# Kernel optimization log

Hardware: AMD Instinct MI355X
Metric: run time of the kernel (lower is better)

## Reference

```python
import jax, jax.numpy as jnp
import numpy as np
from jax import lax

GAMMA = 1.0
INF = 1000000.0  # matches the TF code's pseudo-infinity


def _pairwise_sq_dists(a, b):
    # ||a_i - b_j||^2 = ||a||^2 + ||b||^2 - 2 a.b ; avoids the [B,N,M,d] diff tensor
    a2 = jnp.sum(a * a, axis=-1)                      # (B, N)
    b2 = jnp.sum(b * b, axis=-1)                      # (B, M)
    ab = jnp.einsum('bnd,bmd->bnm', a, b)             # (B, N, M)
    return a2[:, :, None] + b2[:, None, :] - 2.0 * ab


def _soft_dtw(seq_a, seq_b, gamma):
    D = _pairwise_sq_dists(seq_a, seq_b)              # (B, N, M)
    B, N, M = D.shape
    dtype = D.dtype
    # row 0 of the DP table: R[0,0]=0, R[0,j>0]=INF
    row0 = jnp.full((B, M + 1), INF, dtype=dtype).at[:, 0].set(0.0)

    def row_step(prev_row, d_i):
        # prev_row: (B, M+1) = R[i-1, :]; d_i: (B, M) = D[:, i-1, :]
        def col_step(left, inputs):
            diag, up, d = inputs                      # each (B,)
            r = jnp.stack([diag, up, left], axis=-1)  # (B, 3)
            softmin = -gamma * jax.nn.logsumexp(-r / gamma, axis=-1)
            val = d + softmin
            return val, val
        left0 = jnp.full((B,), INF, dtype=dtype)      # R[i, 0] = INF
        xs = (prev_row[:, :-1].T, prev_row[:, 1:].T, d_i.T)  # scan over M
        _, vals = lax.scan(col_step, left0, xs)       # (M, B)
        new_row = jnp.concatenate([jnp.full((B, 1), INF, dtype=dtype), vals.T], axis=1)
        return new_row, None

    final_row, _ = lax.scan(row_step, row0, jnp.moveaxis(D, 1, 0))
    return final_row[:, -1]                           # R[N, M]


def setup_inputs() -> dict:
    key = jax.random.key(0)
    k1, k2 = jax.random.split(key)
    B, N, M, d = 128, 384, 384, 128
    seq_a = jax.random.normal(k1, (B, N, d), dtype=jnp.float32)
    seq_b = jax.random.normal(k2, (B, M, d), dtype=jnp.float32)
    return {"seq_a": seq_a, "seq_b": seq_b}


def reference(seq_a, seq_b):
    dist = _soft_dtw(seq_a, seq_b, GAMMA)
    return dist[:, None]                              # (B, 1)
```

## Files before the change

### kernel.cpp

```cpp
#include <hip/hip_runtime.h>
#include <stdint.h>

#define BATCH 128
#define SEQN  384
#define SEQM  384
#define DIM   128
#define KINF   1000000.0f
#define LOG2E  1.4426950408889634f
#define LN2    0.6931471805599453f
#define KINF2  (KINF * LOG2E)

#define RING    204
#define RSTRIDE 392

#define EXP2F(x) __builtin_amdgcn_exp2f(x)
#define LOG2F(x) __builtin_amdgcn_logf(x)

#define WG __HIP_MEMORY_SCOPE_WORKGROUP

typedef __attribute__((ext_vector_type(8))) short bf16x8;
typedef __attribute__((ext_vector_type(4))) float f32x4;

__device__ __forceinline__ unsigned short bf16_rne(float x) {
    uint32_t u = __float_as_uint(x);
    u += 0x7FFFu + ((u >> 16) & 1u);
    return (unsigned short)(u >> 16);
}
__device__ __forceinline__ uint32_t bf16_pair(float x, float y) {
    uint32_t ux = __float_as_uint(x); ux += 0x7FFFu + ((ux >> 16) & 1u);
    uint32_t uy = __float_as_uint(y); uy += 0x7FFFu + ((uy >> 16) & 1u);
    return (ux >> 16) | (uy & 0xFFFF0000u);
}

union frag_u { bf16x8 v; uint32_t u[4]; };

__global__ __launch_bounds__(512) void fused_dtw(
        const float* __restrict__ A, const float* __restrict__ B,
        float* __restrict__ out) {
    __shared__ __align__(16) unsigned short ring[RING * RSTRIDE];
    __shared__ __align__(16) float normA[SEQN];
    __shared__ int prod_done[16];
    __shared__ int cons_pp;

    const int bat  = blockIdx.x;
    const int tid  = threadIdx.x;
    const int wv   = tid >> 6;
    const int lane = tid & 63;

    if (tid < 16) prod_done[tid] = 0;
    if (tid == 16) cons_pp = -1;
    __syncthreads();

    if (wv == 4) {
        int g = 0;
        while (__hip_atomic_load(&cons_pp, __ATOMIC_ACQUIRE, WG) < 84) {
            __builtin_amdgcn_s_sleep(8);
            if (++g > (1 << 20)) break;
        }
        uint32_t pv = bf16_pair(KINF2, KINF2);
        #pragma unroll
        for (int c = 0; c < 4; c++) {
            uint32_t* p = (uint32_t*)&ring[(384 - RING + c) * RSTRIDE + 6 * lane];
            p[0] = pv; p[1] = pv; p[2] = pv;
        }
        if (lane == 0)
            __hip_atomic_fetch_add(&prod_done[12], 6, __ATOMIC_RELEASE, WG);
        return;
    }

    if (wv != 0) {
        const int pidx  = (wv < 4) ? (wv - 1) : (wv - 2);
        const int sbase = pidx * 4;
        const int l16 = lane & 15, q = lane >> 4;
        const float* __restrict__ Ab = A + (long)bat * SEQN * DIM;
        const float* __restrict__ Bb = B + (long)bat * SEQM * DIM;
        bool first = true;
        for (int k = 0; k < 12; k++) {
            if (k >= 6) {
                int thr = 8 * k - 12, g = 0;
                while (__hip_atomic_load(&cons_pp, __ATOMIC_ACQUIRE, WG) < thr) {
                    __builtin_amdgcn_s_sleep(2);
                    if (++g > (1 << 21)) break;
                }
            }
            frag_u bfrag[2][4];
            float bn[2];
            #pragma unroll
            for (int jg = 0; jg < 2; jg++) {
                const float* bp = Bb + (long)(32 * k + jg * 16 + l16) * DIM + q * 8;
                float s = 0.0f;
                #pragma unroll
                for (int kk = 0; kk < 4; kk++) {
                    float4 v0 = *(const float4*)(bp + kk * 32);
                    float4 v1 = *(const float4*)(bp + kk * 32 + 4);
                    bfrag[jg][kk].u[0] = bf16_pair(v0.x, v0.y);
                    bfrag[jg][kk].u[1] = bf16_pair(v0.z, v0.w);
                    bfrag[jg][kk].u[2] = bf16_pair(v1.x, v1.y);
                    bfrag[jg][kk].u[3] = bf16_pair(v1.z, v1.w);
                    s += v0.x*v0.x + v0.y*v0.y + v0.z*v0.z + v0.w*v0.w
                       + v1.x*v1.x + v1.y*v1.y + v1.z*v1.z + v1.w*v1.w;
                }
                s += __shfl_xor(s, 16, 64);
                s += __shfl_xor(s, 32, 64);
                bn[jg] = s;
            }
            float4 c0v[4], c1v[4];
            {
                const float* ap = Ab + (long)(sbase * 16 + l16) * DIM + q * 8;
                #pragma unroll
                for (int kk = 0; kk < 4; kk++) {
                    c0v[kk] = *(const float4*)(ap + kk * 32);
                    c1v[kk] = *(const float4*)(ap + kk * 32 + 4);
                }
            }
            #pragma unroll
            for (int s4 = 0; s4 < 4; s4++) {
                const int si = sbase + s4;
                float4 n0[4], n1[4];
                if (s4 < 3) {
                    const float* ap = Ab + (long)((si + 1) * 16 + l16) * DIM + q * 8;
                    #pragma unroll
                    for (int kk = 0; kk < 4; kk++) {
                        n0[kk] = *(const float4*)(ap + kk * 32);
                        n1[kk] = *(const float4*)(ap + kk * 32 + 4);
                    }
                }
                frag_u afr[4];
                #pragma unroll
                for (int kk = 0; kk < 4; kk++) {
                    afr[kk].u[0] = bf16_pair(c0v[kk].x, c0v[kk].y);
                    afr[kk].u[1] = bf16_pair(c0v[kk].z, c0v[kk].w);
                    afr[kk].u[2] = bf16_pair(c1v[kk].x, c1v[kk].y);
                    afr[kk].u[3] = bf16_pair(c1v[kk].z, c1v[kk].w);
                }
                if (first) {
                    float sa = 0.0f;
                    #pragma unroll
                    for (int kk = 0; kk < 4; kk++)
                        sa += c0v[kk].x*c0v[kk].x + c0v[kk].y*c0v[kk].y
                            + c0v[kk].z*c0v[kk].z + c0v[kk].w*c0v[kk].w
                            + c1v[kk].x*c1v[kk].x + c1v[kk].y*c1v[kk].y
                            + c1v[kk].z*c1v[kk].z + c1v[kk].w*c1v[kk].w;
                    sa += __shfl_xor(sa, 16, 64);
                    sa += __shfl_xor(sa, 32, 64);
                    if (q == 0) normA[si * 16 + l16] = sa;
                }
                f32x4 acc0 = {0.0f, 0.0f, 0.0f, 0.0f};
                f32x4 acc1 = {0.0f, 0.0f, 0.0f, 0.0f};
                #pragma unroll
                for (int kk = 0; kk < 4; kk++) {
                    acc0 = __builtin_amdgcn_mfma_f32_16x16x32_bf16(
                               afr[kk].v, bfrag[0][kk].v, acc0, 0, 0, 0);
                    acc1 = __builtin_amdgcn_mfma_f32_16x16x32_bf16(
                               afr[kk].v, bfrag[1][kk].v, acc1, 0, 0, 0);
                }
                if (first) asm volatile("s_waitcnt lgkmcnt(0)" ::: "memory");
                float4 an = *(const float4*)&normA[si * 16 + q * 4];
                #pragma unroll
                for (int jg = 0; jg < 2; jg++) {
                    int col  = 32 * k + jg * 16 + l16;
                    int slot = col >= RING ? col - RING : col;
                    f32x4 ac = jg ? acc1 : acc0;
                    ushort4 pk;
                    pk.x = bf16_rne((an.x + bn[jg] - 2.0f * ac[0]) * LOG2E);
                    pk.y = bf16_rne((an.y + bn[jg] - 2.0f * ac[1]) * LOG2E);
                    pk.z = bf16_rne((an.z + bn[jg] - 2.0f * ac[2]) * LOG2E);
                    pk.w = bf16_rne((an.w + bn[jg] - 2.0f * ac[3]) * LOG2E);
                    *(ushort4*)&ring[slot * RSTRIDE + si * 16 + q * 4] = pk;
                }
                if (s4 < 3) {
                    #pragma unroll
                    for (int kk = 0; kk < 4; kk++) { c0v[kk] = n0[kk]; c1v[kk] = n1[kk]; }
                }
            }
            first = false;
            if (lane == 0)
                __hip_atomic_fetch_add(&prod_done[k], 1, __ATOMIC_RELEASE, WG);
        }
        return;
    }

    const int t = lane;
    {
        int g = 0;
        while (__hip_atomic_load(&prod_done[0], __ATOMIC_ACQUIRE, WG) < 6)
            if (++g > (1 << 22)) break;
    }
    __builtin_amdgcn_s_setprio(1);
    const unsigned short* __restrict__ ringT = ring + 6 * t;

    float prev[6];
    #pragma unroll
    for (int r = 0; r < 6; r++) prev[r] = KINF2;

    uint3 dslot[4];
    #pragma unroll
    for (int qq = 0; qq < 4; qq++) {
        int c = qq - 2 * t;
        int cc = c < 0 ? 0 : c;
        dslot[qq] = *(const uint3*)(ringT + (long)cc * RSTRIDE);
    }

    float rcv0 = KINF2, rcv1 = KINF2, old_diag = KINF2;
    float lane0_diag = 0.0f;
    const bool isl0 = (t == 0);
    int c0 = -2 * t;

#define UNPACK(d, w)                                                        \
    d[0] = __uint_as_float(w.x << 16);                                      \
    d[1] = __uint_as_float(w.x & 0xFFFF0000u);                              \
    d[2] = __uint_as_float(w.y << 16);                                      \
    d[3] = __uint_as_float(w.y & 0xFFFF0000u);                              \
    d[4] = __uint_as_float(w.z << 16);                                      \
    d[5] = __uint_as_float(w.z & 0xFFFF0000u);

#define COLPASS(dX, diag0, upseed, LEFTV, NEWV)                             \
    {                                                                       \
        float Bp = (upseed), Fp = 1.0f;                                     \
        float Bv[6], Fv[6];                                                 \
        _Pragma("unroll")                                                   \
        for (int r = 0; r < 6; r++) {                                       \
            float vd = (r == 0) ? (diag0) : LEFTV[r - 1];                   \
            float vl = LEFTV[r];                                            \
            float m3 = fminf(fminf(vd, vl), Bp);            \
            float al = EXP2F(m3 - Bp);                                      \
            float be = EXP2F(m3 - vd) + EXP2F(m3 - vl);                     \
            float Fr = __builtin_fmaf(al, Fp, be);                          \
            float Br = dX[r] + m3;                                          \
            Bv[r] = Br; Fv[r] = Fr;                                         \
            Bp = Br; Fp = Fr;                                               \
        }                                                                   \
        _Pragma("unroll")                                                   \
        for (int r = 0; r < 6; r++)                                         \
            NEWV[r] = Bv[r] - LOG2F(Fv[r]);                                 \
    }

#define PHASE2(Q)                                                           \
    {                                                                       \
        uint3 wA = dslot[Q];                                                \
        uint3 wB = dslot[(Q) + 1];                                          \
        {            \
            int cnA = c0 + 4;                                               \
            int ccA = cnA < 0 ? 0 : (cnA > 387 ? 387 : cnA);                \
            int sA  = ccA >= RING ? ccA - RING : ccA;                       \
            int cnB = c0 + 5;                                               \
            int ccB = cnB < 0 ? 0 : (cnB > 387 ? 387 : cnB);                \
            int sB  = ccB >= RING ? ccB - RING : ccB;                       \
            dslot[Q]       = *(const uint3*)(ringT + (long)sA * RSTRIDE);   \
            dslot[(Q) + 1] = *(const uint3*)(ringT + (long)sB * RSTRIDE);   \
        }                                                                   \
        float dA[6], dB[6];                                                 \
        UNPACK(dA, wA)                                                      \
        UNPACK(dB, wB)                                                      \
        float dgA = isl0 ? lane0_diag : old_diag;                           \
        float upA = isl0 ? KINF2 : rcv0;                                    \
        float upB = isl0 ? KINF2 : rcv1;                                    \
        float newA[6];                                                      \
        COLPASS(dA, dgA, upA, prev, newA)                                   \
        COLPASS(dB, upA, upB, newA, prev)                                   \
        old_diag = rcv1;                                                    \
        rcv0 = __shfl_up(newA[5], 1, 64);                                   \
        rcv1 = __shfl_up(prev[5], 1, 64);                                   \
        lane0_diag = KINF2;                                                 \
        c0 += 2;                                                            \
    }

    for (int pp = 0; pp < 127; pp++) {
        if ((pp & 7) == 7) {
            int k = (4 * pp + 7) >> 5;
            if (k < 13) {
                int g = 0;
                while (__hip_atomic_load(&prod_done[k], __ATOMIC_ACQUIRE, WG) < 6)
                    if (++g > (1 << 22)) break;
            }
        }
        PHASE2(0)
        PHASE2(2)
        if (t == 0)
            __hip_atomic_store(&cons_pp, pp, __ATOMIC_RELEASE, WG);
    }
    PHASE2(0)
#undef PHASE2
#undef COLPASS
#undef UNPACK

    if (t == 63) out[bat] = prev[5] * LN2;
}

extern "C" void kernel_launch(void* const* d_in, const int* in_sizes, int n_in,
                              void* d_out, int out_size, void* d_ws, size_t ws_size,
                              hipStream_t stream) {
    (void)in_sizes; (void)n_in; (void)out_size; (void)d_ws; (void)ws_size;
    const float* a = (const float*)d_in[0];
    const float* b = (const float*)d_in[1];
    float* out = (float*)d_out;

    fused_dtw<<<dim3(BATCH), dim3(512), 0, stream>>>(a, b, out);
}
```

Before: 199.1 us.

## Reduce consumer wavefront skew to one column per lane

```diff
diff --git a/kernel.cpp b/kernel.cpp
--- a/kernel.cpp
+++ b/kernel.cpp
@@ -40,7 +40,7 @@
     __shared__ __align__(16) unsigned short ring[RING * RSTRIDE];
     __shared__ __align__(16) float normA[SEQN];
     __shared__ int prod_done[16];
-    __shared__ int cons_pp;
+    __shared__ int cons_sl;
 
     const int bat  = blockIdx.x;
     const int tid  = threadIdx.x;
@@ -48,12 +48,12 @@
     const int lane = tid & 63;
 
     if (tid < 16) prod_done[tid] = 0;
-    if (tid == 16) cons_pp = -1;
+    if (tid == 16) cons_sl = -1;
     __syncthreads();
 
     if (wv == 4) {
         int g = 0;
-        while (__hip_atomic_load(&cons_pp, __ATOMIC_ACQUIRE, WG) < 84) {
+        while (__hip_atomic_load(&cons_sl, __ATOMIC_ACQUIRE, WG) < 248) {
             __builtin_amdgcn_s_sleep(8);
             if (++g > (1 << 20)) break;
         }
@@ -77,8 +77,8 @@
         bool first = true;
         for (int k = 0; k < 12; k++) {
             if (k >= 6) {
-                int thr = 8 * k - 12, g = 0;
-                while (__hip_atomic_load(&cons_pp, __ATOMIC_ACQUIRE, WG) < thr) {
+                int thr = 32 * k - 110, g = 0;
+                while (__hip_atomic_load(&cons_sl, __ATOMIC_ACQUIRE, WG) < thr) {
                     __builtin_amdgcn_s_sleep(2);
                     if (++g > (1 << 21)) break;
                 }
@@ -195,16 +195,16 @@
 
     uint3 dslot[4];
     #pragma unroll
-    for (int qq = 0; qq < 4; qq++) {
-        int c = qq - 2 * t;
+    for (int j = 0; j < 4; j++) {
+        int c = j - t;
         int cc = c < 0 ? 0 : c;
-        dslot[qq] = *(const uint3*)(ringT + (long)cc * RSTRIDE);
-    }
-
-    float rcv0 = KINF2, rcv1 = KINF2, old_diag = KINF2;
+        dslot[j] = *(const uint3*)(ringT + (long)cc * RSTRIDE);
+    }
+
+    float rcv_up = KINF2, rcv_diag = KINF2;
     float lane0_diag = 0.0f;
     const bool isl0 = (t == 0);
-    int c0 = -2 * t;
+    int kdone = 0;
 
 #define UNPACK(d, w)                                                        \
     d[0] = __uint_as_float(w.x << 16);                                      \
@@ -235,52 +235,45 @@
             NEWV[r] = Bv[r] - LOG2F(Fv[r]);                                 \
     }
 
-#define PHASE2(Q)                                                           \
+#define SLOT(J, S)                                                          \
     {                                                                       \
-        uint3 wA = dslot[Q];                                                \
-        uint3 wB = dslot[(Q) + 1];                                          \
-        {            \
-            int cnA = c0 + 4;                                               \
-            int ccA = cnA < 0 ? 0 : (cnA > 387 ? 387 : cnA);                \
-            int sA  = ccA >= RING ? ccA - RING : ccA;                       \
-            int cnB = c0 + 5;                                               \
-            int ccB = cnB < 0 ? 0 : (cnB > 387 ? 387 : cnB);                \
-            int sB  = ccB >= RING ? ccB - RING : ccB;                       \
-            dslot[Q]       = *(const uint3*)(ringT + (long)sA * RSTRIDE);   \
-            dslot[(Q) + 1] = *(const uint3*)(ringT + (long)sB * RSTRIDE);   \
+        uint3 w = dslot[J];                                                 \
+        {   int cn = (S) + 4 - t;                                           \
+            int cc = cn < 0 ? 0 : (cn > 387 ? 387 : cn);                    \
+            int sl = cc >= RING ? cc - RING : cc;                           \
+            dslot[J] = *(const uint3*)(ringT + (long)sl * RSTRIDE);         \
         }                                                                   \
-        float dA[6], dB[6];                                                 \
-        UNPACK(dA, wA)                                                      \
-        UNPACK(dB, wB)                                                      \
-        float dgA = isl0 ? lane0_diag : old_diag;                           \
-        float upA = isl0 ? KINF2 : rcv0;                                    \
-        float upB = isl0 ? KINF2 : rcv1;                                    \
-        float newA[6];                                                      \
-        COLPASS(dA, dgA, upA, prev, newA)                                   \
-        COLPASS(dB, upA, upB, newA, prev)                                   \
-        old_diag = rcv1;                                                    \
-        rcv0 = __shfl_up(newA[5], 1, 64);                                   \
-        rcv1 = __shfl_up(prev[5], 1, 64);                                   \
+        float d6[6];                                                        \
+        UNPACK(d6, w)                                                       \
+        float dg = isl0 ? lane0_diag : rcv_diag;                            \
+        float up = isl0 ? KINF2 : rcv_up;                                   \
+        COLPASS(d6, dg, up, prev, prev)                                     \
+        rcv_diag = rcv_up;                                                  \
+        rcv_up = __shfl_up(prev[5], 1, 64);                                 \
         lane0_diag = KINF2;                                                 \
-        c0 += 2;                                                            \
-    }
-
-    for (int pp = 0; pp < 127; pp++) {
-        if ((pp & 7) == 7) {
-            int k = (4 * pp + 7) >> 5;
-            if (k < 13) {
-                int g = 0;
-                while (__hip_atomic_load(&prod_done[k], __ATOMIC_ACQUIRE, WG) < 6)
-                    if (++g > (1 << 22)) break;
-            }
-        }
-        PHASE2(0)
-        PHASE2(2)
-        if (t == 0)
-            __hip_atomic_store(&cons_pp, pp, __ATOMIC_RELEASE, WG);
-    }
-    PHASE2(0)
-#undef PHASE2
+    }
+
+    for (int i = 0; i < 111; i++) {
+        int kr = (4 * i + 7) >> 5;
+        if (kr > 12) kr = 12;
+        if (kr > kdone) {
+            int g = 0;
+            while (__hip_atomic_load(&prod_done[kr], __ATOMIC_ACQUIRE, WG) < 6)
+                if (++g > (1 << 22)) break;
+            kdone = kr;
+        }
+        SLOT(0, 4 * i)
+        SLOT(1, 4 * i + 1)
+        SLOT(2, 4 * i + 2)
+        SLOT(3, 4 * i + 3)
+        if ((i & 1) && t == 0)
+            __hip_atomic_store(&cons_sl, 4 * i + 3,
+                               __ATOMIC_RELEASE, WG);
+    }
+    SLOT(0, 444)
+    SLOT(1, 445)
+    SLOT(2, 446)
+#undef SLOT
 #undef COLPASS
 #undef UNPACK
 
```

After: 186.9 us. 1.06x faster.
